# Kernel tuning notes

Measured on AMD Instinct MI355X. Metric: run time of the kernel, lower is better.

## Reference

```python
import jax, jax.numpy as jnp
import numpy as np

NUM = 21  # classes 1..NUM scored; bin 0 is background, bin NUM+1 is a dump bin


def _class_counts(y_pred, y_true):
    # Single-pass histogram over all classes instead of O(num) full-tensor scans.
    yp = y_pred.ravel()
    yt = y_true.ravel()
    nbins = NUM + 2
    cnt_true = jnp.zeros((nbins,), jnp.float32).at[yt].add(1.0)
    cnt_pred = jnp.zeros((nbins,), jnp.float32).at[yp].add(1.0)
    # intersection: positions where pred == true, binned by label; mismatches -> dump bin
    inter_idx = jnp.where(yp == yt, yt, NUM + 1)
    inter = jnp.zeros((nbins,), jnp.float32).at[inter_idx].add(1.0)
    return cnt_true, cnt_pred, inter


def setup_inputs() -> dict:
    key = jax.random.key(0)
    k1, k2 = jax.random.split(key)
    shape = (32, 1024, 1024)
    y_pred = jax.random.randint(k1, shape, 0, NUM + 1, dtype=jnp.int32)
    y_true = jax.random.randint(k2, shape, 0, NUM + 1, dtype=jnp.int32)
    return {"y_pred": y_pred, "y_true": y_true}


def reference(y_pred, y_true):
    cnt_true, cnt_pred, inter = _class_counts(y_pred, y_true)
    # classes 1..NUM (label 0 skipped, as in the original loop over range(1, num+1))
    c_true = cnt_true[1:NUM + 1]
    c_pred = cnt_pred[1:NUM + 1]
    c_inter = inter[1:NUM + 1]
    union = c_true + c_pred - c_inter
    iou = (c_inter + 1e-6) / (union + 1e-6)  # [NUM]
    present = (c_true > 0).astype(jnp.float32)
    mIoU = jnp.sum(iou * present) / jnp.maximum(jnp.sum(present), 1.0)
    return mIoU, iou
```

## Files before the change

### kernel.cpp

```cpp
#include <hip/hip_runtime.h>


#define NUMC   21
#define NBINS  22
#define NCNT   (3 * NBINS)
#define REPS   32
#define RSTRIDE 67

__global__ void zero_counters(unsigned int* __restrict__ g) {
    int i = threadIdx.x;
    if (i < NCNT) g[i] = 0u;
}

__global__ void __launch_bounds__(256) hist_kernel(
        const int* __restrict__ yp, const int* __restrict__ yt,
        unsigned int* __restrict__ g, int n) {
    __shared__ unsigned int h[REPS * RSTRIDE];
    for (int i = threadIdx.x; i < REPS * RSTRIDE; i += blockDim.x) h[i] = 0u;
    __syncthreads();

    unsigned int* hh = h + (threadIdx.x >> 3) * RSTRIDE;

    const int n4 = n >> 2;
    const int4* __restrict__ yp4 = (const int4*)yp;
    const int4* __restrict__ yt4 = (const int4*)yt;
    int tid = blockIdx.x * blockDim.x + threadIdx.x;
    int stride = gridDim.x * blockDim.x;

    for (int i = tid; i < n4; i += stride) {
        int4 p = yp4[i];
        int4 t = yt4[i];
#define PROC(P, T)                                        \
        do {                                              \
            atomicAdd(&hh[(T)], 1u);                      \
            atomicAdd(&hh[NBINS + (P)], 1u);              \
            if ((P) == (T)) atomicAdd(&hh[2*NBINS + (T)], 1u); \
        } while (0)
        PROC(p.x, t.x);
        PROC(p.y, t.y);
        PROC(p.z, t.z);
        PROC(p.w, t.w);
#undef PROC
    }

    if (tid == 0) {
        for (int i = n4 << 2; i < n; i++) {
            int p = yp[i], t = yt[i];
            atomicAdd(&g[t], 1u);
            atomicAdd(&g[NBINS + p], 1u);
            if (p == t) atomicAdd(&g[2*NBINS + t], 1u);
        }
    }

    __syncthreads();
    for (int i = threadIdx.x; i < NCNT; i += blockDim.x) {
        unsigned int s = 0;
        #pragma unroll
        for (int r = 0; r < REPS; r++) s += h[r * RSTRIDE + i];
        atomicAdd(&g[i], s);
    }
}

__global__ void finalize_kernel(const unsigned int* __restrict__ g,
                                float* __restrict__ out) {
    int lane = threadIdx.x;
    float iou = 0.0f, pres = 0.0f;
    if (lane < NUMC) {
        int c = lane + 1;
        float ct = (float)g[c];
        float cp = (float)g[NBINS + c];
        float ci = (float)g[2 * NBINS + c];
        float uni = ct + cp - ci;
        iou = (ci + 1e-6f) / (uni + 1e-6f);
        pres = (ct > 0.0f) ? 1.0f : 0.0f;
        out[1 + lane] = iou;
    }
    float v = iou * pres;
    float p = pres;
    #pragma unroll
    for (int off = 32; off > 0; off >>= 1) {
        v += __shfl_down(v, off);
        p += __shfl_down(p, off);
    }
    if (lane == 0) out[0] = v / fmaxf(p, 1.0f);
}

extern "C" void kernel_launch(void* const* d_in, const int* in_sizes, int n_in,
                              void* d_out, int out_size, void* d_ws, size_t ws_size,
                              hipStream_t stream) {
    const int* yp = (const int*)d_in[0];
    const int* yt = (const int*)d_in[1];
    int n = in_sizes[0];
    unsigned int* g = (unsigned int*)d_ws;
    float* out = (float*)d_out;

    zero_counters<<<1, 128, 0, stream>>>(g);
    hist_kernel<<<2048, 256, 0, stream>>>(yp, yt, g, n);
    finalize_kernel<<<1, 64, 0, stream>>>(g, out);
}
```

Before: 292.3 us.

## Replace three marginal histograms with one joint confusion-matrix histogram

Each element now does a single LDS atomic into a 22x22 joint (true,pred) histogram instead of up to three atomics into separate true/pred/intersection histograms. The marginals and the diagonal are recovered in the finalize kernel. Per-block partials are written to workspace and summed by a separate reduction kernel, which drops the global atomics and the zeroing kernel. LDS replication falls from 32 copies to 4 (one per wavefront), so contention on each copy rises, and there is an extra launch plus partial-buffer traffic.

```diff
diff --git a/kernel.cpp b/kernel.cpp
--- a/kernel.cpp
+++ b/kernel.cpp
@@ -1,88 +1,91 @@
 #include <hip/hip_runtime.h>
 
 
-#define NUMC   21
-#define NBINS  22
-#define NCNT   (3 * NBINS)
-#define REPS   32
-#define RSTRIDE 67
+#define NUMC  21
+#define NBINS 22
+#define JBINS (NBINS * NBINS)
+#define RSTR  485
+#define NREP  4
 
-__global__ void zero_counters(unsigned int* __restrict__ g) {
-    int i = threadIdx.x;
-    if (i < NCNT) g[i] = 0u;
-}
-
-__global__ void __launch_bounds__(256) hist_kernel(
+__global__ void __launch_bounds__(256) hist_joint(
         const int* __restrict__ yp, const int* __restrict__ yt,
-        unsigned int* __restrict__ g, int n) {
-    __shared__ unsigned int h[REPS * RSTRIDE];
-    for (int i = threadIdx.x; i < REPS * RSTRIDE; i += blockDim.x) h[i] = 0u;
+        unsigned int* __restrict__ partials, int n, int nblocks) {
+    __shared__ unsigned int h[NREP * RSTR];
+    for (int i = threadIdx.x; i < NREP * RSTR; i += 256) h[i] = 0u;
     __syncthreads();
 
-    unsigned int* hh = h + (threadIdx.x >> 3) * RSTRIDE;
+    unsigned int* hh = h + (threadIdx.x >> 6) * RSTR;
 
-    const int n4 = n >> 2;
     const int4* __restrict__ yp4 = (const int4*)yp;
     const int4* __restrict__ yt4 = (const int4*)yt;
-    int tid = blockIdx.x * blockDim.x + threadIdx.x;
-    int stride = gridDim.x * blockDim.x;
+    const int n4 = n >> 2;
+    int tid = blockIdx.x * 256 + threadIdx.x;
+    int stride = nblocks * 256;
 
     for (int i = tid; i < n4; i += stride) {
         int4 p = yp4[i];
         int4 t = yt4[i];
-#define PROC(P, T)                                        \
-        do {                                              \
-            atomicAdd(&hh[(T)], 1u);                      \
-            atomicAdd(&hh[NBINS + (P)], 1u);              \
-            if ((P) == (T)) atomicAdd(&hh[2*NBINS + (T)], 1u); \
-        } while (0)
-        PROC(p.x, t.x);
-        PROC(p.y, t.y);
-        PROC(p.z, t.z);
-        PROC(p.w, t.w);
-#undef PROC
+        atomicAdd(&hh[t.x * NBINS + p.x], 1u);
+        atomicAdd(&hh[t.y * NBINS + p.y], 1u);
+        atomicAdd(&hh[t.z * NBINS + p.z], 1u);
+        atomicAdd(&hh[t.w * NBINS + p.w], 1u);
     }
 
     if (tid == 0) {
-        for (int i = n4 << 2; i < n; i++) {
-            int p = yp[i], t = yt[i];
-            atomicAdd(&g[t], 1u);
-            atomicAdd(&g[NBINS + p], 1u);
-            if (p == t) atomicAdd(&g[2*NBINS + t], 1u);
-        }
+        for (int i = n4 << 2; i < n; i++)
+            atomicAdd(&hh[yt[i] * NBINS + yp[i]], 1u);
     }
 
     __syncthreads();
-    for (int i = threadIdx.x; i < NCNT; i += blockDim.x) {
+    for (int c = threadIdx.x; c < JBINS; c += 256) {
         unsigned int s = 0;
         #pragma unroll
-        for (int r = 0; r < REPS; r++) s += h[r * RSTRIDE + i];
-        atomicAdd(&g[i], s);
+        for (int r = 0; r < NREP; r++) s += h[r * RSTR + c];
+        partials[(size_t)blockIdx.x * JBINS + c] = s;
     }
+}
+
+__global__ void __launch_bounds__(256) reduce_partials(
+        const unsigned int* __restrict__ partials,
+        unsigned int* __restrict__ g, int nblocks) {
+    __shared__ unsigned int lds[256];
+    const int c = blockIdx.x;
+    unsigned int s = 0;
+    for (int b = threadIdx.x; b < nblocks; b += 256)
+        s += partials[(size_t)b * JBINS + c];
+    lds[threadIdx.x] = s;
+    __syncthreads();
+    for (int w = 128; w > 0; w >>= 1) {
+        if (threadIdx.x < w) lds[threadIdx.x] += lds[threadIdx.x + w];
+        __syncthreads();
+    }
+    if (threadIdx.x == 0) g[c] = lds[0];
 }
 
 __global__ void finalize_kernel(const unsigned int* __restrict__ g,
                                 float* __restrict__ out) {
     int lane = threadIdx.x;
     float iou = 0.0f, pres = 0.0f;
-    if (lane < NUMC) {
-        int c = lane + 1;
-        float ct = (float)g[c];
-        float cp = (float)g[NBINS + c];
-        float ci = (float)g[2 * NBINS + c];
-        float uni = ct + cp - ci;
-        iou = (ci + 1e-6f) / (uni + 1e-6f);
-        pres = (ct > 0.0f) ? 1.0f : 0.0f;
-        out[1 + lane] = iou;
+    if (lane >= 1 && lane <= NUMC) {
+        unsigned int ct = 0, cp = 0;
+        #pragma unroll
+        for (int k = 0; k < NBINS; k++) {
+            ct += g[lane * NBINS + k];
+            cp += g[k * NBINS + lane];
+        }
+        unsigned int ci = g[lane * NBINS + lane];
+        float u = (float)ct + (float)cp - (float)ci;
+        iou = ((float)ci + 1e-6f) / (u + 1e-6f);
+        pres = (ct > 0u) ? 1.0f : 0.0f;
+        out[lane] = iou;
     }
-    float v = iou * pres;
-    float p = pres;
+    float v = iou * pres, pc = pres;
     #pragma unroll
     for (int off = 32; off > 0; off >>= 1) {
         v += __shfl_down(v, off);
-        p += __shfl_down(p, off);
+        pc += __shfl_down(pc, off);
     }
-    if (lane == 0) out[0] = v / fmaxf(p, 1.0f);
+    if (lane == 0) out[0] = v / fmaxf(pc, 1.0f);
 }
 
 extern "C" void kernel_launch(void* const* d_in, const int* in_sizes, int n_in,
@@ -91,10 +94,14 @@
     const int* yp = (const int*)d_in[0];
     const int* yt = (const int*)d_in[1];
     int n = in_sizes[0];
-    unsigned int* g = (unsigned int*)d_ws;
     float* out = (float*)d_out;
 
-    zero_counters<<<1, 128, 0, stream>>>(g);
-    hist_kernel<<<2048, 256, 0, stream>>>(yp, yt, g, n);
+    int nb = 2048;
+    while (nb > 1 && (size_t)JBINS * 4 * ((size_t)nb + 1) > ws_size) nb >>= 1;
+    unsigned int* g = (unsigned int*)d_ws;
+    unsigned int* partials = g + JBINS;
+
+    hist_joint<<<nb, 256, 0, stream>>>(yp, yt, partials, n, nb);
+    reduce_partials<<<JBINS, 256, 0, stream>>>(partials, g, nb);
     finalize_kernel<<<1, 64, 0, stream>>>(g, out);
 }
```

After: 285.2 us. 2.4% less time.
